# Kernel optimization log

Measured on AMD Instinct MI355X. Metric: run time of the kernel, lower is better.

## Reference

```python
import jax, jax.numpy as jnp
import numpy as np

B, T, F, H = 64, 512, 512, 1024


def setup_inputs() -> dict:
    key = jax.random.key(0)
    k1, k2, k3 = jax.random.split(key, 3)
    x = jax.random.normal(k1, (B, T, F), dtype=jnp.float32)
    c0 = jnp.zeros((B, H), dtype=jnp.float32)
    h0 = jnp.zeros((B, H), dtype=jnp.float32)
    # Flax LSTMCell: input projection (no bias) + hidden projection (with bias),
    # fused here into [4H]-wide kernels with gate order (i, f, g, o).
    Wi = jax.random.normal(k2, (F, 4 * H), dtype=jnp.float32) / np.sqrt(F)
    Wh = jax.random.normal(k3, (H, 4 * H), dtype=jnp.float32) / np.sqrt(H)
    bh = jnp.zeros((4 * H,), dtype=jnp.float32)
    return {"x": x, "c0": c0, "h0": h0, "Wi": Wi, "Wh": Wh, "bh": bh}


def reference(x, c0, h0, Wi, Wh, bh):
    # Precompute input projections for the whole sequence in one big GEMM.
    # zx: (T, B, 4H)
    zx = jnp.einsum('btf,fg->tbg', x, Wi)

    def step(carry, zx_t):
        c, h = carry
        z = zx_t + h @ Wh + bh  # (B, 4H)
        i, f, g, o = jnp.split(z, 4, axis=-1)
        i = jax.nn.sigmoid(i)
        f = jax.nn.sigmoid(f)
        g = jnp.tanh(g)
        o = jax.nn.sigmoid(o)
        c_new = f * c + i * g
        h_new = o * jnp.tanh(c_new)
        return (c_new, h_new), h_new

    (_, _), ys = jax.lax.scan(step, (c0, h0), zx)
    return jnp.swapaxes(ys, 0, 1)  # (B, T, H)
```

## Files before the change

kernel.cpp:

```cpp
#include <hip/hip_runtime.h>

#define Bdim 64
#define Tdim 512
#define Fdim 512
#define Hdim 1024
#define NKB  48
#define NXKB 16
#define NHKB 32
#define NWG  128
#define NTHR 512

typedef __attribute__((ext_vector_type(8))) _Float16     f16x8;
typedef __attribute__((ext_vector_type(4))) float        f32x4;
typedef __attribute__((ext_vector_type(4))) unsigned int u32x4;

#define MFMA(a, b, c) __builtin_amdgcn_mfma_f32_16x16x32_f16((a), (b), (c), 0, 0, 0)

#define WP_ELEMS    (256*48*64*8)
#define BIAS_OFF    ((size_t)WP_ELEMS * 2)
#define HBUF_OFF    (BIAS_OFF + 4096 * 4)
#define SLOT_BYTES  131072
#define NRING       513
#define FLAG_OFF    (HBUF_OFF + (size_t)NRING * SLOT_BYTES)
#define FLAG_STRIDE 32

__device__ __forceinline__ float sigmoidf_(float v) {
    return 1.0f / (1.0f + __expf(-v));
}
__device__ __forceinline__ float tanhf_(float v) {
    return 1.0f - 2.0f / (1.0f + __expf(2.0f * v));
}

__device__ __forceinline__ f16x8 uload16_l2(const void* p) {
    f16x8 r;
    asm volatile("global_load_dwordx4 %0, %1, off sc0"
                 : "=v"(r) : "v"(p) : "memory");
    return r;
}
__device__ __forceinline__ void ustore16(void* p, f32x4 v) {
    asm volatile("global_store_dwordx4 %0, %1, off sc0 sc1"
                 :: "v"(p), "v"(v) : "memory");
}

#define WAITV(N) do { asm volatile("s_waitcnt vmcnt(" #N ")" ::: "memory"); \
                      __builtin_amdgcn_sched_barrier(0); } while (0)

__device__ __forceinline__ unsigned ldtok(const unsigned* p) {
    return __hip_atomic_load(p, __ATOMIC_RELAXED, __HIP_MEMORY_SCOPE_WORKGROUP);
}
__device__ __forceinline__ void sttok(unsigned* p, unsigned v) {
    __hip_atomic_store(p, v, __ATOMIC_RELAXED, __HIP_MEMORY_SCOPE_WORKGROUP);
}

__global__ void pack_w_kernel(const float* __restrict__ Wi, const float* __restrict__ Wh,
                              _Float16* __restrict__ Wp)
{
    int d = blockIdx.x * blockDim.x + threadIdx.x;
    int tn   = d / 3072;
    int r    = d % 3072;
    int kb   = r / 64;
    int lane = r % 64;
    int kg = lane >> 4, lm = lane & 15;
    int Np = tn * 16 + lm;
    int g    = Np >> 5;
    int lc   = Np & 31;
    int gate = lc >> 3, c = lc & 7;
    int n  = gate * Hdim + g * 8 + c;
    int k0 = kb * 32 + kg * 8;
    f16x8 v;
#pragma unroll
    for (int j = 0; j < 8; ++j) {
        int k = k0 + j;
        float w = (k < Fdim) ? Wi[(long)k * 4096 + n] : Wh[(long)(k - Fdim) * 4096 + n];
        v[j] = (_Float16)w;
    }
    ((f16x8*)Wp)[d] = v;
}

__global__ void pack_misc_kernel(const float* __restrict__ bh, const float* __restrict__ h0,
                                 float* __restrict__ bias_p, _Float16* __restrict__ hbuf,
                                 unsigned int* __restrict__ flags)
{
    int t = blockIdx.x * blockDim.x + threadIdx.x;
    if (t < NWG) flags[t * FLAG_STRIDE] = 0u;
    if (t < 4096) {
        int g = t >> 5, lc = t & 31;
        int gate = lc >> 3, c = lc & 7;
        bias_p[t] = bh[gate * Hdim + g * 8 + c];
    }
    {
        int wgp = t >> 9;
        int b   = (t >> 3) & 63;
        int c   = t & 7;
        hbuf[t] = (_Float16)h0[b * Hdim + wgp * 8 + c];
    }
}

__global__ __launch_bounds__(NTHR, 1)
void lstm_kernel(const float* __restrict__ x, const float* __restrict__ c0,
                 const f16x8* __restrict__ Wp8, const float* __restrict__ bias_p,
                 _Float16* __restrict__ hbuf, unsigned int* __restrict__ flags,
                 float* __restrict__ out)
{
    __shared__ f16x8 wlds[2 * NKB * 64];
    __shared__ float zlds[Bdim][33];
    __shared__ float zxlds[2][Bdim][33];
    __shared__ unsigned gateT[4];
    __shared__ unsigned prodDone[4];
    __shared__ unsigned consDone[4];

    const int wg    = (blockIdx.x & 7) * 16 + (blockIdx.x >> 3);
    const int tid   = threadIdx.x;
    const int wave  = tid >> 6;
    const int lane  = tid & 63;
    const int kg    = lane >> 4;
    const int lm    = lane & 15;
    const bool isH  = (wave < 4);
    const int  rt   = isH ? wave : (wave - 4);

    {
        const f16x8* src = Wp8 + (size_t)wg * 2 * NKB * 64;
        for (int e = tid; e < 2 * NKB * 64; e += NTHR) wlds[e] = src[e];
    }
    if (tid < 4) { gateT[tid] = 0; prodDone[tid] = 0; consDone[tid] = 0; }

    const float bias0 = bias_p[wg * 32 + lm];
    const float bias1 = bias_p[wg * 32 + 16 + lm];

    const int grow = (wave & 3) * 16 + (lane >> 2);
    const int gjl  = (lane & 3) * 2;
    float cc0 = 0.f, cc1 = 0.f;
    if (isH) {
        cc0 = c0[grow * Hdim + wg * 8 + gjl];
        cc1 = c0[grow * Hdim + wg * 8 + gjl + 1];
    }

    const int arow = rt * 16 + lm;
    const float* __restrict__ xrow = x + (size_t)arow * Tdim * Fdim + kg * 8;

    char* __restrict__ hb  = (char*)hbuf;
    const char* __restrict__ hrd = hb + (size_t)kg * 1024 + (size_t)arow * 16;
    const size_t mypkt = (size_t)wg * 1024 + (size_t)grow * 16;

#define XPHASE(TT, BUF)                                                     \
    {                                                                       \
        const float* xt = xrow + (size_t)(TT) * Fdim;                       \
        f32x4 xa0 = {0.f, 0.f, 0.f, 0.f};                                   \
        f32x4 xa1 = {0.f, 0.f, 0.f, 0.f};                                   \
        _Pragma("unroll 8")                                                 \
        for (int kb = 0; kb < NXKB; ++kb) {                                 \
            const f32x4* ap = (const f32x4*)(xt + kb * 32);                 \
            f32x4 lo = ap[0];                                               \
            f32x4 hi = ap[1];                                               \
            f16x8 a;                                                        \
            _Pragma("unroll")                                               \
            for (int j = 0; j < 4; ++j) { a[j] = (_Float16)lo[j]; a[4+j] = (_Float16)hi[j]; } \
            xa0 = MFMA(a, wlds[kb * 64 + lane], xa0);                       \
            xa1 = MFMA(a, wlds[NKB * 64 + kb * 64 + lane], xa1);            \
        }                                                                   \
        int rbase = rt * 16 + kg * 4;                                       \
        _Pragma("unroll")                                                   \
        for (int r = 0; r < 4; ++r) {                                       \
            zxlds[BUF][rbase + r][lm]      = xa0[r];                        \
            zxlds[BUF][rbase + r][16 + lm] = xa1[r];                        \
        }                                                                   \
    }

    if (!isH) XPHASE(0, 0);
    __syncthreads();
    if (!isH && lane == 0) sttok(&prodDone[rt], 1u);

    for (int t = 0; t < Tdim; ++t) {
        if (isH) {
            f32x4 acc0a = {bias0, bias0, bias0, bias0};
            f32x4 acc1a = {bias1, bias1, bias1, bias1};
            f32x4 acc0b = {0.f, 0.f, 0.f, 0.f};
            f32x4 acc1b = {0.f, 0.f, 0.f, 0.f};
            {
                const char* hq = hrd + (size_t)t * SLOT_BYTES;
                f16x8 hA[8], hB[8], hC[8], hD[8];

#define HGATE(G)                                                        \
                if (t) { while (ldtok(&gateT[G]) < (unsigned)t)         \
                             __builtin_amdgcn_s_sleep(1); }

#define HLOAD(BASE, H)                                                  \
                _Pragma("unroll")                                       \
                for (int k = 0; k < 8; ++k)                             \
                    H[k] = uload16_l2(hq + (size_t)((BASE) + k) * 4096);

#define HGROUP(BASE, H)                                                 \
                _Pragma("unroll")                                       \
                for (int k = 0; k < 8; ++k) {                           \
                    int kb = (BASE) + k;                                \
                    f16x8 bf0 = wlds[(NXKB + kb) * 64 + lane];          \
                    f16x8 bf1 = wlds[NKB * 64 + (NXKB + kb) * 64 + lane]; \
                    if (kb & 1) { acc0b = MFMA(H[k], bf0, acc0b); acc1b = MFMA(H[k], bf1, acc1b); } \
                    else        { acc0a = MFMA(H[k], bf0, acc0a); acc1a = MFMA(H[k], bf1, acc1a); } \
                }

                HGATE(0); HLOAD(0,  hA);
                HGATE(1); HLOAD(8,  hB);
                WAITV(8);
                HGROUP(0,  hA);
                HGATE(2); HLOAD(16, hC);
                WAITV(8);
                HGROUP(8,  hB);
                HGATE(3); HLOAD(24, hD);
                WAITV(8);
                HGROUP(16, hC);
                WAITV(0);
                HGROUP(24, hD);
#undef HGATE
#undef HLOAD
#undef HGROUP
            }
            {
                while (ldtok(&prodDone[rt]) < (unsigned)(t + 1))
                    __builtin_amdgcn_s_sleep(1);
                const int buf = t & 1;
                int rbase = rt * 16 + kg * 4;
#pragma unroll
                for (int r = 0; r < 4; ++r) {
                    float z0 = acc0a[r] + acc0b[r] + zxlds[buf][rbase + r][lm];
                    float z1 = acc1a[r] + acc1b[r] + zxlds[buf][rbase + r][16 + lm];
                    zlds[rbase + r][lm]      = z0;
                    zlds[rbase + r][16 + lm] = z1;
                }
            }
            asm volatile("s_waitcnt lgkmcnt(0)" ::: "memory");
            __builtin_amdgcn_sched_barrier(0);
            if (lane == 0) sttok(&consDone[rt], (unsigned)(t + 1));

            float hv0, hv1;
            {
                float i0 = sigmoidf_(zlds[grow][gjl]);
                float f0 = sigmoidf_(zlds[grow][8 + gjl]);
                float g0 = tanhf_(zlds[grow][16 + gjl]);
                float o0 = sigmoidf_(zlds[grow][24 + gjl]);
                cc0 = f0 * cc0 + i0 * g0;
                hv0 = o0 * tanhf_(cc0);

                float i1 = sigmoidf_(zlds[grow][gjl + 1]);
                float f1 = sigmoidf_(zlds[grow][8 + gjl + 1]);
                float g1 = tanhf_(zlds[grow][16 + gjl + 1]);
                float o1 = sigmoidf_(zlds[grow][24 + gjl + 1]);
                cc1 = f1 * cc1 + i1 * g1;
                hv1 = o1 * tanhf_(cc1);
            }

            {
                union { _Float16 h[2]; unsigned int u; } pk;
                pk.h[0] = (_Float16)hv0; pk.h[1] = (_Float16)hv1;
                const int lb = lane & ~3;
                unsigned int q0 = __shfl(pk.u, lb);
                unsigned int q1 = __shfl(pk.u, lb + 1);
                unsigned int q2 = __shfl(pk.u, lb + 2);
                unsigned int q3 = __shfl(pk.u, lb + 3);
                if (!(lane & 3)) {
                    u32x4 pkt = {q0, q1, q2, q3};
                    ustore16(hb + (size_t)(t + 1) * SLOT_BYTES + mypkt,
                             __builtin_bit_cast(f32x4, pkt));
                }
            }
            WAITV(0);
            if (lane == 0)
                __hip_atomic_fetch_add(flags + (size_t)wg * FLAG_STRIDE, 1u,
                                       __ATOMIC_RELAXED, __HIP_MEMORY_SCOPE_AGENT);
            {
                float2 ov; ov.x = hv0; ov.y = hv1;
                *(float2*)(out + ((size_t)grow * Tdim + t) * Hdim + wg * 8 + gjl) = ov;
            }
        } else {
            {
                if (t) {
                    while (ldtok(&consDone[rt]) < (unsigned)t)
                        __builtin_amdgcn_s_sleep(1);
                }
                const int tn  = (t + 1 < Tdim) ? (t + 1) : t;
                const int buf = (t + 1) & 1;
                XPHASE(tn, buf);
            }
            asm volatile("s_waitcnt lgkmcnt(0)" ::: "memory");
            if (lane == 0) sttok(&prodDone[rt], (unsigned)(t + 2));

            if (wave == 4 && t + 1 < Tdim) {
                const unsigned tgt = 4u * (unsigned)(t + 1);
                unsigned posted = 0;
                while (posted != 0xFu) {
                    unsigned f0 = __hip_atomic_load(flags + (size_t)lane * FLAG_STRIDE,
                                                    __ATOMIC_RELAXED, __HIP_MEMORY_SCOPE_AGENT);
                    unsigned f1 = __hip_atomic_load(flags + (size_t)(64 + lane) * FLAG_STRIDE,
                                                    __ATOMIC_RELAXED, __HIP_MEMORY_SCOPE_AGENT);
                    unsigned long long b0 = __ballot(f0 >= tgt);
                    unsigned long long b1 = __ballot(f1 >= tgt);
                    if (!(posted & 1u) && (unsigned)b0 == 0xFFFFFFFFu) {
                        if (lane == 0) sttok(&gateT[0], (unsigned)(t + 1));
                        posted |= 1u;
                    }
                    if (!(posted & 2u) && (unsigned)(b0 >> 32) == 0xFFFFFFFFu) {
                        if (lane == 0) sttok(&gateT[1], (unsigned)(t + 1));
                        posted |= 2u;
                    }
                    if (!(posted & 4u) && (unsigned)b1 == 0xFFFFFFFFu) {
                        if (lane == 0) sttok(&gateT[2], (unsigned)(t + 1));
                        posted |= 4u;
                    }
                    if (!(posted & 8u) && (unsigned)(b1 >> 32) == 0xFFFFFFFFu) {
                        if (lane == 0) sttok(&gateT[3], (unsigned)(t + 1));
                        posted |= 8u;
                    }
                    if (posted != 0xFu) __builtin_amdgcn_s_sleep(1);
                }
            }
        }
    }
#undef XPHASE
}

extern "C" void kernel_launch(void* const* d_in, const int* in_sizes, int n_in,
                              void* d_out, int out_size, void* d_ws, size_t ws_size,
                              hipStream_t stream)
{
    const float* x  = (const float*)d_in[0];
    const float* c0 = (const float*)d_in[1];
    const float* h0 = (const float*)d_in[2];
    const float* Wi = (const float*)d_in[3];
    const float* Wh = (const float*)d_in[4];
    const float* bh = (const float*)d_in[5];
    float* out = (float*)d_out;

    char* ws = (char*)d_ws;
    _Float16*     Wp     = (_Float16*)(ws);
    float*        bias_p = (float*)(ws + BIAS_OFF);
    _Float16*     hbuf   = (_Float16*)(ws + HBUF_OFF);
    unsigned int* flags  = (unsigned int*)(ws + FLAG_OFF);

    hipLaunchKernelGGL(pack_w_kernel,    dim3(3072), dim3(256), 0, stream, Wi, Wh, Wp);
    hipLaunchKernelGGL(pack_misc_kernel, dim3(256),  dim3(256), 0, stream, bh, h0, bias_p, hbuf, flags);
    hipLaunchKernelGGL(lstm_kernel, dim3(NWG), dim3(NTHR), 0, stream,
                       x, c0, (const f16x8*)Wp, bias_p, hbuf, flags, out);
}
```

Measured before the change: 3.147 ms.

## Pre-fill h ring with sentinels and drop producer store-wait before flag

Fills every h ring slot after the first with an all-ones sentinel before the LSTM kernel runs. Consumers check each loaded h fragment for the sentinel and re-load with cache bypass until real data arrives. This lets producers bump their ready flag without first waiting for the h store to complete. The flag round trip moves off the critical path. The cost is an extra 64 MB fill kernel per call and sentinel checks in the inner loop. It also relies on real fp16 h pairs never matching 0xFFFFFFFF, which would be a NaN pattern.

```diff
diff --git a/kernel.cpp b/kernel.cpp
--- a/kernel.cpp
+++ b/kernel.cpp
@@ -37,6 +37,12 @@
                  : "=v"(r) : "v"(p) : "memory");
     return r;
 }
+__device__ __forceinline__ f16x8 uload16_byp(const void* p) {
+    f16x8 r;
+    asm volatile("global_load_dwordx4 %0, %1, off sc0 sc1"
+                 : "=v"(r) : "v"(p) : "memory");
+    return r;
+}
 __device__ __forceinline__ void ustore16(void* p, f32x4 v) {
     asm volatile("global_store_dwordx4 %0, %1, off sc0 sc1"
                  :: "v"(p), "v"(v) : "memory");
@@ -44,6 +50,12 @@
 
 #define WAITV(N) do { asm volatile("s_waitcnt vmcnt(" #N ")" ::: "memory"); \
                       __builtin_amdgcn_sched_barrier(0); } while (0)
+
+__device__ __forceinline__ bool stale8(f16x8 v) {
+    u32x4 u = __builtin_bit_cast(u32x4, v);
+    return (u[0] == 0xFFFFFFFFu) | (u[1] == 0xFFFFFFFFu) |
+           (u[2] == 0xFFFFFFFFu) | (u[3] == 0xFFFFFFFFu);
+}
 
 __device__ __forceinline__ unsigned ldtok(const unsigned* p) {
     return __hip_atomic_load(p, __ATOMIC_RELAXED, __HIP_MEMORY_SCOPE_WORKGROUP);
@@ -75,6 +87,13 @@
         v[j] = (_Float16)w;
     }
     ((f16x8*)Wp)[d] = v;
+}
+
+__global__ void pack_ring_kernel(_Float16* __restrict__ hbuf)
+{
+    size_t i = (size_t)blockIdx.x * 256 + threadIdx.x;
+    u32x4 sv = {0xFFFFFFFFu, 0xFFFFFFFFu, 0xFFFFFFFFu, 0xFFFFFFFFu};
+    *(u32x4*)((char*)hbuf + SLOT_BYTES + i * 16) = sv;
 }
 
 __global__ void pack_misc_kernel(const float* __restrict__ bh, const float* __restrict__ h0,
@@ -189,6 +208,22 @@
                 for (int k = 0; k < 8; ++k)                             \
                     H[k] = uload16_l2(hq + (size_t)((BASE) + k) * 4096);
 
+#define HCHECK(BASE, H)                                                 \
+                {                                                       \
+                    bool st[8]; bool any = false;                       \
+                    _Pragma("unroll")                                   \
+                    for (int k = 0; k < 8; ++k) { st[k] = stale8(H[k]); any |= st[k]; } \
+                    while (__any(any)) {                                \
+                        _Pragma("unroll")                               \
+                        for (int k = 0; k < 8; ++k)                     \
+                            if (st[k]) H[k] = uload16_byp(hq + (size_t)((BASE) + k) * 4096); \
+                        WAITV(0);                                       \
+                        any = false;                                    \
+                        _Pragma("unroll")                               \
+                        for (int k = 0; k < 8; ++k) { st[k] = stale8(H[k]); any |= st[k]; } \
+                    }                                                   \
+                }
+
 #define HGROUP(BASE, H)                                                 \
                 _Pragma("unroll")                                       \
                 for (int k = 0; k < 8; ++k) {                           \
@@ -202,17 +237,18 @@
                 HGATE(0); HLOAD(0,  hA);
                 HGATE(1); HLOAD(8,  hB);
                 WAITV(8);
-                HGROUP(0,  hA);
+                HCHECK(0,  hA);  HGROUP(0,  hA);
                 HGATE(2); HLOAD(16, hC);
                 WAITV(8);
-                HGROUP(8,  hB);
+                HCHECK(8,  hB);  HGROUP(8,  hB);
                 HGATE(3); HLOAD(24, hD);
                 WAITV(8);
-                HGROUP(16, hC);
+                HCHECK(16, hC);  HGROUP(16, hC);
                 WAITV(0);
-                HGROUP(24, hD);
+                HCHECK(24, hD);  HGROUP(24, hD);
 #undef HGATE
 #undef HLOAD
+#undef HCHECK
 #undef HGROUP
             }
             {
@@ -263,7 +299,6 @@
                              __builtin_bit_cast(f32x4, pkt));
                 }
             }
-            WAITV(0);
             if (lane == 0)
                 __hip_atomic_fetch_add(flags + (size_t)wg * FLAG_STRIDE, 1u,
                                        __ATOMIC_RELAXED, __HIP_MEMORY_SCOPE_AGENT);
@@ -336,8 +371,9 @@
     _Float16*     hbuf   = (_Float16*)(ws + HBUF_OFF);
     unsigned int* flags  = (unsigned int*)(ws + FLAG_OFF);
 
-    hipLaunchKernelGGL(pack_w_kernel,    dim3(3072), dim3(256), 0, stream, Wi, Wh, Wp);
-    hipLaunchKernelGGL(pack_misc_kernel, dim3(256),  dim3(256), 0, stream, bh, h0, bias_p, hbuf, flags);
+    hipLaunchKernelGGL(pack_w_kernel,    dim3(3072),  dim3(256), 0, stream, Wi, Wh, Wp);
+    hipLaunchKernelGGL(pack_ring_kernel, dim3(16384), dim3(256), 0, stream, hbuf);
+    hipLaunchKernelGGL(pack_misc_kernel, dim3(256),   dim3(256), 0, stream, bh, h0, bias_p, hbuf, flags);
     hipLaunchKernelGGL(lstm_kernel, dim3(NWG), dim3(NTHR), 0, stream,
                        x, c0, (const f16x8*)Wp, bias_p, hbuf, flags, out);
 }
```

Measured after the change: 3.571 ms. 1.13x slower.
